# Performance work log

Hardware: AMD Instinct MI355X
Metric: run time of the kernel (lower is better)

## Reference

```python
import jax, jax.numpy as jnp
import numpy as np

DIM = 512
HEADS = 8
WS = 8  # window_size


def setup_inputs() -> dict:
    key = jax.random.key(0)
    ks = jax.random.split(key, 7)
    b, c, h, w = 4, DIM, 192, 192
    x = jax.random.normal(ks[0], (b, c, h, w), dtype=jnp.float32)
    # conv1x1 weights are [out, in] matrices (kernel dim squeezed)
    wq = jax.random.normal(ks[1], (DIM, DIM), dtype=jnp.float32) * 0.02
    wk = jax.random.normal(ks[2], (DIM, DIM), dtype=jnp.float32) * 0.02
    wv = jax.random.normal(ks[3], (DIM, DIM), dtype=jnp.float32) * 0.02
    wo = jax.random.normal(ks[4], (DIM, DIM), dtype=jnp.float32) * 0.02
    bo = jax.random.normal(ks[5], (DIM,), dtype=jnp.float32) * 0.02
    # learned per-head additive bias over window tokens (trunc_normal std=0.02)
    beta = jax.random.normal(ks[6], (HEADS, WS * WS, WS * WS), dtype=jnp.float32) * 0.02
    return {"x": x, "wq": wq, "wk": wk, "wv": wv, "wo": wo, "bo": bo, "beta": beta}


def reference(x, wq, wk, wv, wo, bo, beta):
    b, c, h, w = x.shape
    s = WS
    pad_r = (-w) % s
    pad_b = (-h) % s
    x = jnp.pad(x, ((0, 0), (0, 0), (0, pad_b), (0, pad_r)))
    H, W = h + pad_b, w + pad_r
    nh, nw = H // s, W // s
    n = s * s
    head_dim = c // HEADS
    scale = head_dim ** -0.5
    # window partition: (b, c, nh, s, nw, s) -> (b*nh*nw, c, n)
    xw = x.reshape(b, c, nh, s, nw, s).transpose(0, 2, 4, 1, 3, 5).reshape(b * nh * nw, c, n)
    B = xw.shape[0]
    q = jnp.einsum('oc,bcn->bon', wq, xw).reshape(B, HEADS, head_dim, n)
    k = jnp.einsum('oc,bcn->bon', wk, xw).reshape(B, HEADS, head_dim, n)
    v = jnp.einsum('oc,bcn->bon', wv, xw).reshape(B, HEADS, head_dim, n)
    attn = jnp.einsum('bhdn,bhdm->bhnm', q, k) * scale + beta  # [B,H,n,n]
    attn = jax.nn.softmax(attn, axis=-1)
    o = jnp.einsum('bhnm,bhdm->bhdn', attn, v).reshape(B, c, n)
    o = jnp.einsum('oc,bcn->bon', wo, o) + bo[None, :, None]
    # window merge back to image
    out = o.reshape(b, nh, nw, c, s, s).transpose(0, 3, 1, 4, 2, 5).reshape(b, c, H, W)
    return out[:, :, :h, :w]
```

## Files before the change

### kernel.cpp

```cpp
#include <hip/hip_runtime.h>

typedef unsigned short ushort_t;
typedef __attribute__((ext_vector_type(4))) float f32x4;
typedef __attribute__((ext_vector_type(8))) short short8;

__device__ __forceinline__ ushort_t f2bf(float f) {
  union { float f; unsigned u; } v; v.f = f;
  unsigned r = v.u + 0x7fffu + ((v.u >> 16) & 1u);
  return (ushort_t)(r >> 16);
}

__global__ __launch_bounds__(256) void cvt_w_k(const float* __restrict__ wq,
                                               const float* __restrict__ wk,
                                               const float* __restrict__ wv,
                                               const float* __restrict__ wo,
                                               ushort_t* __restrict__ dst) {
  int idx = (blockIdx.x * 256 + threadIdx.x) * 4;
  int m = idx >> 18;
  int off = idx & 0x3ffff;
  const float* s = (m == 0) ? wq : (m == 1) ? wk : (m == 2) ? wv : wo;
  float4 v = *(const float4*)(s + off);
  ushort4 o;
  o.x = f2bf(v.x); o.y = f2bf(v.y); o.z = f2bf(v.z); o.w = f2bf(v.w);
  *(ushort4*)(dst + idx) = o;
}

__global__ __launch_bounds__(256) void xpose_k(const float* __restrict__ x,
                                               ushort_t* __restrict__ xT) {
  __shared__ ushort_t tile[128 * 80];
  int bid = blockIdx.x;
  int win = bid >> 2, kc = bid & 3;
  int b = win / 576, rem = win % 576, wh = rem / 24, ww = rem % 24;
  int tid = threadIdx.x;
  {
    int c_l = tid >> 1, half = tid & 1;
    const float* xb = x + (((b * 512 + kc * 128 + c_l) * 192 + wh * 8) * 192 + ww * 8);
#pragma unroll
    for (int ii = 0; ii < 4; ++ii) {
      int i = half * 4 + ii;
      float4 v0 = *(const float4*)(xb + i * 192);
      float4 v1 = *(const float4*)(xb + i * 192 + 4);
      uint4 u;
      u.x = (unsigned)f2bf(v0.x) | ((unsigned)f2bf(v0.y) << 16);
      u.y = (unsigned)f2bf(v0.z) | ((unsigned)f2bf(v0.w) << 16);
      u.z = (unsigned)f2bf(v1.x) | ((unsigned)f2bf(v1.y) << 16);
      u.w = (unsigned)f2bf(v1.z) | ((unsigned)f2bf(v1.w) << 16);
      *(uint4*)&tile[c_l * 80 + i * 8] = u;
    }
  }
  __syncthreads();
  {
    int tok = tid >> 2, q = tid & 3;
    unsigned w[16];
#pragma unroll
    for (int k = 0; k < 16; ++k) {
      unsigned lo = tile[(q * 32 + 2 * k) * 80 + tok];
      unsigned hi = tile[(q * 32 + 2 * k + 1) * 80 + tok];
      w[k] = lo | (hi << 16);
    }
    ushort_t* d = xT + ((win * 64 + tok) * 512 + kc * 128 + q * 32);
#pragma unroll
    for (int s2 = 0; s2 < 4; ++s2) {
      uint4 u; u.x = w[s2 * 4 + 0]; u.y = w[s2 * 4 + 1]; u.z = w[s2 * 4 + 2]; u.w = w[s2 * 4 + 3];
      *(uint4*)(d + s2 * 8) = u;
    }
  }
}

__global__ __launch_bounds__(256) void attn_k(const ushort_t* __restrict__ xT,
                                              const ushort_t* __restrict__ wB,
                                              const float* __restrict__ beta,
                                              ushort_t* __restrict__ Og) {
  __shared__ ushort_t xws[64 * 136];
  __shared__ ushort_t qTs[64 * 72];
  __shared__ ushort_t kTs[64 * 72];
  __shared__ ushort_t vSs[64 * 72];
  int bid = blockIdx.x;
  int win = bid >> 3, h = bid & 7;
  int tid = threadIdx.x, lane = tid & 63, wid = tid >> 6;
  int l15 = lane & 15, l4 = lane >> 4;
  int t0 = win * 64;
  const ushort_t* wqh = wB + (h * 64) * 512;
  const ushort_t* wkh = wB + 262144 + (h * 64) * 512;
  const ushort_t* wvh = wB + 524288 + (h * 64) * 512;

  f32x4 z = {0.f, 0.f, 0.f, 0.f};
  f32x4 aq[4], ak[4], av[4];
#pragma unroll
  for (int i = 0; i < 4; ++i) { aq[i] = z; ak[i] = z; av[i] = z; }

  int stok = tid >> 2, sq = tid & 3;
  int dcol = wid * 16 + l15;
  for (int kcc = 0; kcc < 4; ++kcc) {
    {
      const uint4* src = (const uint4*)(xT + ((t0 + stok) * 512 + kcc * 128 + sq * 32));
      uint4* dstv = (uint4*)&xws[stok * 136 + sq * 32];
#pragma unroll
      for (int s2 = 0; s2 < 4; ++s2) dstv[s2] = src[s2];
    }
    __syncthreads();
#pragma unroll
    for (int kk = 0; kk < 4; ++kk) {
      int cg = kcc * 128 + kk * 32 + l4 * 8;
      short8 bq = *(const short8*)(wqh + dcol * 512 + cg);
      short8 bk = *(const short8*)(wkh + dcol * 512 + cg);
      short8 bv = *(const short8*)(wvh + dcol * 512 + cg);
#pragma unroll
      for (int nt = 0; nt < 4; ++nt) {
        short8 a = *(const short8*)&xws[(nt * 16 + l15) * 136 + kk * 32 + l4 * 8];
        aq[nt] = __builtin_amdgcn_mfma_f32_16x16x32_bf16(a, bq, aq[nt], 0, 0, 0);
        ak[nt] = __builtin_amdgcn_mfma_f32_16x16x32_bf16(a, bk, ak[nt], 0, 0, 0);
        av[nt] = __builtin_amdgcn_mfma_f32_16x16x32_bf16(a, bv, av[nt], 0, 0, 0);
      }
    }
    __syncthreads();
  }
#pragma unroll
  for (int nt = 0; nt < 4; ++nt) {
#pragma unroll
    for (int r = 0; r < 4; ++r) {
      int n = nt * 16 + l4 * 4 + r;
      int d = wid * 16 + l15;
      qTs[n * 72 + d] = f2bf(aq[nt][r]);
      kTs[n * 72 + d] = f2bf(ak[nt][r]);
    }
    uint2 u;
    u.x = (unsigned)f2bf(av[nt][0]) | ((unsigned)f2bf(av[nt][1]) << 16);
    u.y = (unsigned)f2bf(av[nt][2]) | ((unsigned)f2bf(av[nt][3]) << 16);
    *(uint2*)&vSs[(wid * 16 + l15) * 72 + nt * 16 + l4 * 4] = u;
  }
  __syncthreads();

  f32x4 sA[4];
#pragma unroll
  for (int i = 0; i < 4; ++i) sA[i] = z;
#pragma unroll
  for (int kk = 0; kk < 2; ++kk) {
    short8 aF = *(const short8*)&qTs[(wid * 16 + l15) * 72 + kk * 32 + l4 * 8];
#pragma unroll
    for (int mt = 0; mt < 4; ++mt) {
      short8 bF = *(const short8*)&kTs[(mt * 16 + l15) * 72 + kk * 32 + l4 * 8];
      sA[mt] = __builtin_amdgcn_mfma_f32_16x16x32_bf16(aF, bF, sA[mt], 0, 0, 0);
    }
  }
  const float* betah = beta + h * 4096;
  float p[4][4];
  float rmax[4] = {-1e30f, -1e30f, -1e30f, -1e30f};
#pragma unroll
  for (int mt = 0; mt < 4; ++mt)
#pragma unroll
    for (int r = 0; r < 4; ++r) {
      int n = wid * 16 + l4 * 4 + r;
      float val = sA[mt][r] * 0.125f + betah[n * 64 + mt * 16 + l15];
      p[mt][r] = val;
      rmax[r] = fmaxf(rmax[r], val);
    }
#pragma unroll
  for (int m = 1; m <= 8; m <<= 1)
#pragma unroll
    for (int r = 0; r < 4; ++r) rmax[r] = fmaxf(rmax[r], __shfl_xor(rmax[r], m, 64));
  float rsum[4] = {0.f, 0.f, 0.f, 0.f};
#pragma unroll
  for (int mt = 0; mt < 4; ++mt)
#pragma unroll
    for (int r = 0; r < 4; ++r) {
      p[mt][r] = __expf(p[mt][r] - rmax[r]);
      rsum[r] += p[mt][r];
    }
#pragma unroll
  for (int m = 1; m <= 8; m <<= 1)
#pragma unroll
    for (int r = 0; r < 4; ++r) rsum[r] += __shfl_xor(rsum[r], m, 64);
  float rinv[4];
#pragma unroll
  for (int r = 0; r < 4; ++r) rinv[r] = 1.f / rsum[r];
#pragma unroll
  for (int mt = 0; mt < 4; ++mt)
#pragma unroll
    for (int r = 0; r < 4; ++r)
      qTs[(wid * 16 + l4 * 4 + r) * 72 + mt * 16 + l15] = f2bf(p[mt][r] * rinv[r]);
  __syncthreads();

  f32x4 oA[4];
#pragma unroll
  for (int i = 0; i < 4; ++i) oA[i] = z;
#pragma unroll
  for (int kk = 0; kk < 2; ++kk) {
    short8 aF = *(const short8*)&qTs[(wid * 16 + l15) * 72 + kk * 32 + l4 * 8];
#pragma unroll
    for (int dt = 0; dt < 4; ++dt) {
      short8 bF = *(const short8*)&vSs[(dt * 16 + l15) * 72 + kk * 32 + l4 * 8];
      oA[dt] = __builtin_amdgcn_mfma_f32_16x16x32_bf16(aF, bF, oA[dt], 0, 0, 0);
    }
  }
#pragma unroll
  for (int dt = 0; dt < 4; ++dt)
#pragma unroll
    for (int r = 0; r < 4; ++r) {
      int n = wid * 16 + l4 * 4 + r;
      Og[(t0 + n) * 512 + h * 64 + dt * 16 + l15] = f2bf(oA[dt][r]);
    }
}

__global__ __launch_bounds__(256) void proj_k(const ushort_t* __restrict__ Og,
                                              const ushort_t* __restrict__ woB,
                                              const float* __restrict__ bo,
                                              float* __restrict__ out) {
  __shared__ ushort_t ows[64 * 136];
  int bid = blockIdx.x;
  int win = bid >> 1, mo = (bid & 1) * 256;
  int b = win / 576, rem = win % 576, wh = rem / 24, ww = rem % 24;
  int tid = threadIdx.x, lane = tid & 63, wid = tid >> 6;
  int l15 = lane & 15, l4 = lane >> 4;
  int t0 = win * 64;
  f32x4 z = {0.f, 0.f, 0.f, 0.f};
  f32x4 acc[4][4];
#pragma unroll
  for (int i = 0; i < 4; ++i)
#pragma unroll
    for (int j = 0; j < 4; ++j) acc[i][j] = z;
  int stok = tid >> 2, sq = tid & 3;
  for (int kcc = 0; kcc < 4; ++kcc) {
    {
      const uint4* src = (const uint4*)(Og + ((t0 + stok) * 512 + kcc * 128 + sq * 32));
      uint4* dstv = (uint4*)&ows[stok * 136 + sq * 32];
#pragma unroll
      for (int s2 = 0; s2 < 4; ++s2) dstv[s2] = src[s2];
    }
    __syncthreads();
#pragma unroll
    for (int kk = 0; kk < 4; ++kk) {
      short8 bF[4];
#pragma unroll
      for (int nt = 0; nt < 4; ++nt)
        bF[nt] = *(const short8*)&ows[(nt * 16 + l15) * 136 + kk * 32 + l4 * 8];
      int cg = kcc * 128 + kk * 32 + l4 * 8;
#pragma unroll
      for (int mt = 0; mt < 4; ++mt) {
        int orow = mo + wid * 64 + mt * 16 + l15;
        short8 aF = *(const short8*)(woB + orow * 512 + cg);
#pragma unroll
        for (int nt = 0; nt < 4; ++nt)
          acc[mt][nt] = __builtin_amdgcn_mfma_f32_16x16x32_bf16(aF, bF[nt], acc[mt][nt], 0, 0, 0);
      }
    }
    __syncthreads();
  }
#pragma unroll
  for (int mt = 0; mt < 4; ++mt) {
#pragma unroll
    for (int r = 0; r < 4; ++r) {
      int o = mo + wid * 64 + mt * 16 + l4 * 4 + r;
      float bias = bo[o];
#pragma unroll
      for (int nt = 0; nt < 4; ++nt) {
        int tok = nt * 16 + l15;
        int i = tok >> 3, j = tok & 7;
        out[((b * 512 + o) * 192 + wh * 8 + i) * 192 + ww * 8 + j] = acc[mt][nt][r] + bias;
      }
    }
  }
}

extern "C" void kernel_launch(void* const* d_in, const int* in_sizes, int n_in,
                              void* d_out, int out_size, void* d_ws, size_t ws_size,
                              hipStream_t stream) {
  const float* x    = (const float*)d_in[0];
  const float* wq   = (const float*)d_in[1];
  const float* wk   = (const float*)d_in[2];
  const float* wv   = (const float*)d_in[3];
  const float* wo   = (const float*)d_in[4];
  const float* bo   = (const float*)d_in[5];
  const float* beta = (const float*)d_in[6];

  ushort_t* wB = (ushort_t*)d_ws;
  ushort_t* Og = (ushort_t*)((char*)d_ws + (size_t)4 * 262144 * 2);
  ushort_t* xT = (ushort_t*)d_out;

  cvt_w_k<<<1024, 256, 0, stream>>>(wq, wk, wv, wo, wB);
  xpose_k<<<2304 * 4, 256, 0, stream>>>(x, xT);
  attn_k<<<2304 * 8, 256, 0, stream>>>(xT, wB, beta, Og);
  proj_k<<<2304 * 2, 256, 0, stream>>>(Og, wB + 3 * 262144, bo, (float*)d_out);
}
```

Before: 1.024 ms.

## Process all heads per window in one block, loading window activations once

```diff
diff --git a/kernel.cpp b/kernel.cpp
--- a/kernel.cpp
+++ b/kernel.cpp
@@ -67,139 +67,143 @@
   }
 }
 
-__global__ __launch_bounds__(256) void attn_k(const ushort_t* __restrict__ xT,
-                                              const ushort_t* __restrict__ wB,
-                                              const float* __restrict__ beta,
-                                              ushort_t* __restrict__ Og) {
-  __shared__ ushort_t xws[64 * 136];
-  __shared__ ushort_t qTs[64 * 72];
-  __shared__ ushort_t kTs[64 * 72];
-  __shared__ ushort_t vSs[64 * 72];
-  int bid = blockIdx.x;
-  int win = bid >> 3, h = bid & 7;
+__global__ __launch_bounds__(512) void qkv_attn_k(const ushort_t* __restrict__ xT,
+                                                  const ushort_t* __restrict__ wB,
+                                                  const float* __restrict__ beta,
+                                                  ushort_t* __restrict__ Og) {
+  __shared__ ushort_t xws[64 * 520];
+  __shared__ ushort_t qs[2][64 * 72];
+  __shared__ ushort_t ks[2][64 * 72];
+  __shared__ ushort_t vs[2][64 * 72];
+  int win = blockIdx.x;
+  int t0 = win * 64;
   int tid = threadIdx.x, lane = tid & 63, wid = tid >> 6;
   int l15 = lane & 15, l4 = lane >> 4;
-  int t0 = win * 64;
-  const ushort_t* wqh = wB + (h * 64) * 512;
-  const ushort_t* wkh = wB + 262144 + (h * 64) * 512;
-  const ushort_t* wvh = wB + 524288 + (h * 64) * 512;
-
-  f32x4 z = {0.f, 0.f, 0.f, 0.f};
-  f32x4 aq[4], ak[4], av[4];
-#pragma unroll
-  for (int i = 0; i < 4; ++i) { aq[i] = z; ak[i] = z; av[i] = z; }
-
-  int stok = tid >> 2, sq = tid & 3;
-  int dcol = wid * 16 + l15;
-  for (int kcc = 0; kcc < 4; ++kcc) {
-    {
-      const uint4* src = (const uint4*)(xT + ((t0 + stok) * 512 + kcc * 128 + sq * 32));
-      uint4* dstv = (uint4*)&xws[stok * 136 + sq * 32];
-#pragma unroll
-      for (int s2 = 0; s2 < 4; ++s2) dstv[s2] = src[s2];
-    }
-    __syncthreads();
-#pragma unroll
-    for (int kk = 0; kk < 4; ++kk) {
-      int cg = kcc * 128 + kk * 32 + l4 * 8;
-      short8 bq = *(const short8*)(wqh + dcol * 512 + cg);
-      short8 bk = *(const short8*)(wkh + dcol * 512 + cg);
-      short8 bv = *(const short8*)(wvh + dcol * 512 + cg);
+
+  {
+    int token = tid >> 3, cb = (tid & 7) * 64;
+    const uint4* src = (const uint4*)(xT + (size_t)(t0 + token) * 512 + cb);
+    uint4* dst = (uint4*)&xws[token * 520 + cb];
+#pragma unroll
+    for (int s2 = 0; s2 < 8; ++s2) dst[s2] = src[s2];
+  }
+  __syncthreads();
+
+  const f32x4 z = {0.f, 0.f, 0.f, 0.f};
+
+  for (int hcc = 0; hcc < 4; ++hcc) {
+    f32x4 aq[4], ak[4], av[4];
+#pragma unroll
+    for (int i = 0; i < 4; ++i) { aq[i] = z; ak[i] = z; av[i] = z; }
+    int ocol = hcc * 128 + wid * 16 + l15;
+    const ushort_t* wqr = wB + (size_t)ocol * 512;
+    const ushort_t* wkr = wB + 262144 + (size_t)ocol * 512;
+    const ushort_t* wvr = wB + 524288 + (size_t)ocol * 512;
+#pragma unroll
+    for (int kk = 0; kk < 16; ++kk) {
+      int cg = kk * 32 + l4 * 8;
+      short8 bq = *(const short8*)(wqr + cg);
+      short8 bk = *(const short8*)(wkr + cg);
+      short8 bv = *(const short8*)(wvr + cg);
 #pragma unroll
       for (int nt = 0; nt < 4; ++nt) {
-        short8 a = *(const short8*)&xws[(nt * 16 + l15) * 136 + kk * 32 + l4 * 8];
+        short8 a = *(const short8*)&xws[(nt * 16 + l15) * 520 + cg];
         aq[nt] = __builtin_amdgcn_mfma_f32_16x16x32_bf16(a, bq, aq[nt], 0, 0, 0);
         ak[nt] = __builtin_amdgcn_mfma_f32_16x16x32_bf16(a, bk, ak[nt], 0, 0, 0);
         av[nt] = __builtin_amdgcn_mfma_f32_16x16x32_bf16(a, bv, av[nt], 0, 0, 0);
       }
     }
-    __syncthreads();
-  }
-#pragma unroll
-  for (int nt = 0; nt < 4; ++nt) {
-#pragma unroll
-    for (int r = 0; r < 4; ++r) {
-      int n = nt * 16 + l4 * 4 + r;
-      int d = wid * 16 + l15;
-      qTs[n * 72 + d] = f2bf(aq[nt][r]);
-      kTs[n * 72 + d] = f2bf(ak[nt][r]);
-    }
-    uint2 u;
-    u.x = (unsigned)f2bf(av[nt][0]) | ((unsigned)f2bf(av[nt][1]) << 16);
-    u.y = (unsigned)f2bf(av[nt][2]) | ((unsigned)f2bf(av[nt][3]) << 16);
-    *(uint2*)&vSs[(wid * 16 + l15) * 72 + nt * 16 + l4 * 4] = u;
-  }
-  __syncthreads();
-
-  f32x4 sA[4];
-#pragma unroll
-  for (int i = 0; i < 4; ++i) sA[i] = z;
-#pragma unroll
-  for (int kk = 0; kk < 2; ++kk) {
-    short8 aF = *(const short8*)&qTs[(wid * 16 + l15) * 72 + kk * 32 + l4 * 8];
-#pragma unroll
-    for (int mt = 0; mt < 4; ++mt) {
-      short8 bF = *(const short8*)&kTs[(mt * 16 + l15) * 72 + kk * 32 + l4 * 8];
-      sA[mt] = __builtin_amdgcn_mfma_f32_16x16x32_bf16(aF, bF, sA[mt], 0, 0, 0);
-    }
-  }
-  const float* betah = beta + h * 4096;
-  float p[4][4];
-  float rmax[4] = {-1e30f, -1e30f, -1e30f, -1e30f};
-#pragma unroll
-  for (int mt = 0; mt < 4; ++mt)
-#pragma unroll
-    for (int r = 0; r < 4; ++r) {
-      int n = wid * 16 + l4 * 4 + r;
-      float val = sA[mt][r] * 0.125f + betah[n * 64 + mt * 16 + l15];
-      p[mt][r] = val;
-      rmax[r] = fmaxf(rmax[r], val);
-    }
-#pragma unroll
-  for (int m = 1; m <= 8; m <<= 1)
-#pragma unroll
-    for (int r = 0; r < 4; ++r) rmax[r] = fmaxf(rmax[r], __shfl_xor(rmax[r], m, 64));
-  float rsum[4] = {0.f, 0.f, 0.f, 0.f};
-#pragma unroll
-  for (int mt = 0; mt < 4; ++mt)
-#pragma unroll
-    for (int r = 0; r < 4; ++r) {
-      p[mt][r] = __expf(p[mt][r] - rmax[r]);
-      rsum[r] += p[mt][r];
-    }
-#pragma unroll
-  for (int m = 1; m <= 8; m <<= 1)
-#pragma unroll
-    for (int r = 0; r < 4; ++r) rsum[r] += __shfl_xor(rsum[r], m, 64);
-  float rinv[4];
-#pragma unroll
-  for (int r = 0; r < 4; ++r) rinv[r] = 1.f / rsum[r];
-#pragma unroll
-  for (int mt = 0; mt < 4; ++mt)
-#pragma unroll
-    for (int r = 0; r < 4; ++r)
-      qTs[(wid * 16 + l4 * 4 + r) * 72 + mt * 16 + l15] = f2bf(p[mt][r] * rinv[r]);
-  __syncthreads();
-
-  f32x4 oA[4];
-#pragma unroll
-  for (int i = 0; i < 4; ++i) oA[i] = z;
-#pragma unroll
-  for (int kk = 0; kk < 2; ++kk) {
-    short8 aF = *(const short8*)&qTs[(wid * 16 + l15) * 72 + kk * 32 + l4 * 8];
-#pragma unroll
-    for (int dt = 0; dt < 4; ++dt) {
-      short8 bF = *(const short8*)&vSs[(dt * 16 + l15) * 72 + kk * 32 + l4 * 8];
-      oA[dt] = __builtin_amdgcn_mfma_f32_16x16x32_bf16(aF, bF, oA[dt], 0, 0, 0);
-    }
-  }
-#pragma unroll
-  for (int dt = 0; dt < 4; ++dt)
-#pragma unroll
-    for (int r = 0; r < 4; ++r) {
-      int n = wid * 16 + l4 * 4 + r;
-      Og[(t0 + n) * 512 + h * 64 + dt * 16 + l15] = f2bf(oA[dt][r]);
-    }
+    int hw = wid >> 2;
+    int dd = (wid * 16 + l15) & 63;
+#pragma unroll
+    for (int nt = 0; nt < 4; ++nt) {
+#pragma unroll
+      for (int r = 0; r < 4; ++r) {
+        int n = nt * 16 + l4 * 4 + r;
+        qs[hw][n * 72 + dd] = f2bf(aq[nt][r]);
+        ks[hw][n * 72 + dd] = f2bf(ak[nt][r]);
+      }
+      uint2 u;
+      u.x = (unsigned)f2bf(av[nt][0]) | ((unsigned)f2bf(av[nt][1]) << 16);
+      u.y = (unsigned)f2bf(av[nt][2]) | ((unsigned)f2bf(av[nt][3]) << 16);
+      *(uint2*)&vs[hw][dd * 72 + nt * 16 + l4 * 4] = u;
+    }
+    __syncthreads();
+
+    int hh = wid >> 2, rowg = wid & 3;
+    int h = hcc * 2 + hh;
+    f32x4 sA[4];
+#pragma unroll
+    for (int i = 0; i < 4; ++i) sA[i] = z;
+#pragma unroll
+    for (int kk = 0; kk < 2; ++kk) {
+      short8 aF = *(const short8*)&qs[hh][(rowg * 16 + l15) * 72 + kk * 32 + l4 * 8];
+#pragma unroll
+      for (int mt = 0; mt < 4; ++mt) {
+        short8 bF = *(const short8*)&ks[hh][(mt * 16 + l15) * 72 + kk * 32 + l4 * 8];
+        sA[mt] = __builtin_amdgcn_mfma_f32_16x16x32_bf16(aF, bF, sA[mt], 0, 0, 0);
+      }
+    }
+    const float* betah = beta + h * 4096;
+    float p[4][4];
+    float rmax[4] = {-1e30f, -1e30f, -1e30f, -1e30f};
+#pragma unroll
+    for (int mt = 0; mt < 4; ++mt)
+#pragma unroll
+      for (int r = 0; r < 4; ++r) {
+        int n = rowg * 16 + l4 * 4 + r;
+        float val = sA[mt][r] * 0.125f + betah[n * 64 + mt * 16 + l15];
+        p[mt][r] = val;
+        rmax[r] = fmaxf(rmax[r], val);
+      }
+#pragma unroll
+    for (int m = 1; m <= 8; m <<= 1)
+#pragma unroll
+      for (int r = 0; r < 4; ++r) rmax[r] = fmaxf(rmax[r], __shfl_xor(rmax[r], m, 64));
+    float rsum[4] = {0.f, 0.f, 0.f, 0.f};
+#pragma unroll
+    for (int mt = 0; mt < 4; ++mt)
+#pragma unroll
+      for (int r = 0; r < 4; ++r) {
+        p[mt][r] = __expf(p[mt][r] - rmax[r]);
+        rsum[r] += p[mt][r];
+      }
+#pragma unroll
+    for (int m = 1; m <= 8; m <<= 1)
+#pragma unroll
+      for (int r = 0; r < 4; ++r) rsum[r] += __shfl_xor(rsum[r], m, 64);
+    float rinv[4];
+#pragma unroll
+    for (int r = 0; r < 4; ++r) rinv[r] = 1.f / rsum[r];
+    __syncthreads();
+#pragma unroll
+    for (int mt = 0; mt < 4; ++mt)
+#pragma unroll
+      for (int r = 0; r < 4; ++r)
+        qs[hh][(rowg * 16 + l4 * 4 + r) * 72 + mt * 16 + l15] = f2bf(p[mt][r] * rinv[r]);
+    __syncthreads();
+
+    f32x4 oA[4];
+#pragma unroll
+    for (int i = 0; i < 4; ++i) oA[i] = z;
+#pragma unroll
+    for (int kk = 0; kk < 2; ++kk) {
+      short8 aF = *(const short8*)&qs[hh][(rowg * 16 + l15) * 72 + kk * 32 + l4 * 8];
+#pragma unroll
+      for (int dt = 0; dt < 4; ++dt) {
+        short8 bF = *(const short8*)&vs[hh][(dt * 16 + l15) * 72 + kk * 32 + l4 * 8];
+        oA[dt] = __builtin_amdgcn_mfma_f32_16x16x32_bf16(aF, bF, oA[dt], 0, 0, 0);
+      }
+    }
+#pragma unroll
+    for (int dt = 0; dt < 4; ++dt)
+#pragma unroll
+      for (int r = 0; r < 4; ++r) {
+        int n = rowg * 16 + l4 * 4 + r;
+        Og[(size_t)(t0 + n) * 512 + h * 64 + dt * 16 + l15] = f2bf(oA[dt][r]);
+      }
+    __syncthreads();
+  }
 }
 
 __global__ __launch_bounds__(256) void proj_k(const ushort_t* __restrict__ Og,
@@ -279,6 +283,6 @@
 
   cvt_w_k<<<1024, 256, 0, stream>>>(wq, wk, wv, wo, wB);
   xpose_k<<<2304 * 4, 256, 0, stream>>>(x, xT);
-  attn_k<<<2304 * 8, 256, 0, stream>>>(xT, wB, beta, Og);
+  qkv_attn_k<<<2304, 512, 0, stream>>>(xT, wB, beta, Og);
   proj_k<<<2304 * 2, 256, 0, stream>>>(Og, wB + 3 * 262144, bo, (float*)d_out);
 }
```

After: 991.0 us. 1.03x faster.

## Split QKV projection into a large-tile GEMM and batch-chunk the pipeline

Applied to the files above, without the earlier changes.

```diff
diff --git a/kernel.cpp b/kernel.cpp
--- a/kernel.cpp
+++ b/kernel.cpp
@@ -26,15 +26,15 @@
 }
 
 __global__ __launch_bounds__(256) void xpose_k(const float* __restrict__ x,
-                                               ushort_t* __restrict__ xT) {
+                                               ushort_t* __restrict__ xT, int b0) {
   __shared__ ushort_t tile[128 * 80];
   int bid = blockIdx.x;
-  int win = bid >> 2, kc = bid & 3;
-  int b = win / 576, rem = win % 576, wh = rem / 24, ww = rem % 24;
+  int winl = bid >> 2, kc = bid & 3;
+  int b = b0 + winl / 576, rem = winl % 576, wh = rem / 24, ww = rem % 24;
   int tid = threadIdx.x;
   {
     int c_l = tid >> 1, half = tid & 1;
-    const float* xb = x + (((b * 512 + kc * 128 + c_l) * 192 + wh * 8) * 192 + ww * 8);
+    const float* xb = x + ((((size_t)b * 512 + kc * 128 + c_l) * 192 + wh * 8) * 192 + ww * 8);
 #pragma unroll
     for (int ii = 0; ii < 4; ++ii) {
       int i = half * 4 + ii;
@@ -58,7 +58,7 @@
       unsigned hi = tile[(q * 32 + 2 * k + 1) * 80 + tok];
       w[k] = lo | (hi << 16);
     }
-    ushort_t* d = xT + ((win * 64 + tok) * 512 + kc * 128 + q * 32);
+    ushort_t* d = xT + ((size_t)(winl * 64 + tok) * 512 + kc * 128 + q * 32);
 #pragma unroll
     for (int s2 = 0; s2 < 4; ++s2) {
       uint4 u; u.x = w[s2 * 4 + 0]; u.y = w[s2 * 4 + 1]; u.z = w[s2 * 4 + 2]; u.w = w[s2 * 4 + 3];
@@ -67,79 +67,126 @@
   }
 }
 
-__global__ __launch_bounds__(256) void attn_k(const ushort_t* __restrict__ xT,
-                                              const ushort_t* __restrict__ wB,
-                                              const float* __restrict__ beta,
-                                              ushort_t* __restrict__ Og) {
-  __shared__ ushort_t xws[64 * 136];
-  __shared__ ushort_t qTs[64 * 72];
-  __shared__ ushort_t kTs[64 * 72];
-  __shared__ ushort_t vSs[64 * 72];
+__global__ __launch_bounds__(256) void qkv_k(const ushort_t* __restrict__ xT,
+                                             const ushort_t* __restrict__ wB,
+                                             ushort_t* __restrict__ Og) {
+  __shared__ ushort_t As[128 * 72];
+  __shared__ ushort_t Bs[128 * 72];
   int bid = blockIdx.x;
-  int win = bid >> 3, h = bid & 7;
+  int cwg = gridDim.x >> 3;
+  int wg = (bid & 7) * cwg + (bid >> 3);
+  int mt = wg / 12, nt = wg % 12;
+  int t0 = mt * 128;
+  int tid = threadIdx.x, lane = tid & 63, wid = tid >> 6;
+  int wr = wid >> 1, wc = wid & 1;
+  int l15 = lane & 15, l4 = lane >> 4;
+  const ushort_t* Bsrc = wB + (size_t)(nt * 128) * 512;
+
+  const f32x4 z = {0.f, 0.f, 0.f, 0.f};
+  f32x4 acc[4][4];
+#pragma unroll
+  for (int i = 0; i < 4; ++i)
+#pragma unroll
+    for (int j = 0; j < 4; ++j) acc[i][j] = z;
+
+  int srow[4], sslot[4];
+#pragma unroll
+  for (int c = 0; c < 4; ++c) { int u = c * 256 + tid; srow[c] = u >> 3; sslot[c] = u & 7; }
+
+  uint4 ga[4], gb[4];
+#pragma unroll
+  for (int c = 0; c < 4; ++c) {
+    ga[c] = *(const uint4*)&xT[(size_t)(t0 + srow[c]) * 512 + sslot[c] * 8];
+    gb[c] = *(const uint4*)&Bsrc[(size_t)srow[c] * 512 + sslot[c] * 8];
+  }
+
+  for (int ks = 0; ks < 8; ++ks) {
+    __syncthreads();
+#pragma unroll
+    for (int c = 0; c < 4; ++c) {
+      *(uint4*)&As[srow[c] * 72 + sslot[c] * 8] = ga[c];
+      *(uint4*)&Bs[srow[c] * 72 + sslot[c] * 8] = gb[c];
+    }
+    if (ks < 7) {
+      int ko = (ks + 1) * 64;
+#pragma unroll
+      for (int c = 0; c < 4; ++c) {
+        ga[c] = *(const uint4*)&xT[(size_t)(t0 + srow[c]) * 512 + ko + sslot[c] * 8];
+        gb[c] = *(const uint4*)&Bsrc[(size_t)srow[c] * 512 + ko + sslot[c] * 8];
+      }
+    }
+    __syncthreads();
+#pragma unroll
+    for (int kk = 0; kk < 2; ++kk) {
+      short8 aF[4], bF[4];
+#pragma unroll
+      for (int mi = 0; mi < 4; ++mi)
+        aF[mi] = *(const short8*)&As[(wr * 64 + mi * 16 + l15) * 72 + kk * 32 + l4 * 8];
+#pragma unroll
+      for (int ni = 0; ni < 4; ++ni)
+        bF[ni] = *(const short8*)&Bs[(wc * 64 + ni * 16 + l15) * 72 + kk * 32 + l4 * 8];
+#pragma unroll
+      for (int mi = 0; mi < 4; ++mi)
+#pragma unroll
+        for (int ni = 0; ni < 4; ++ni)
+          acc[mi][ni] = __builtin_amdgcn_mfma_f32_16x16x32_bf16(aF[mi], bF[ni], acc[mi][ni], 0, 0, 0);
+    }
+  }
+#pragma unroll
+  for (int mi = 0; mi < 4; ++mi)
+#pragma unroll
+    for (int rr = 0; rr < 4; ++rr) {
+      size_t row = (size_t)(t0 + wr * 64 + mi * 16 + l4 * 4 + rr) * 1536;
+      int cb = nt * 128 + wc * 64 + l15;
+#pragma unroll
+      for (int ni = 0; ni < 4; ++ni)
+        Og[row + cb + ni * 16] = f2bf(acc[mi][ni][rr]);
+    }
+}
+
+__global__ __launch_bounds__(256) void attn2_k(const ushort_t* __restrict__ Og,
+                                               const float* __restrict__ beta,
+                                               ushort_t* __restrict__ O) {
+  __shared__ ushort_t qS[64 * 72], kS[64 * 72], vT[64 * 72], pS[64 * 72];
+  int bid = blockIdx.x;
+  int winl = bid >> 3, h = bid & 7;
+  int t0 = winl * 64;
   int tid = threadIdx.x, lane = tid & 63, wid = tid >> 6;
   int l15 = lane & 15, l4 = lane >> 4;
-  int t0 = win * 64;
-  const ushort_t* wqh = wB + (h * 64) * 512;
-  const ushort_t* wkh = wB + 262144 + (h * 64) * 512;
-  const ushort_t* wvh = wB + 524288 + (h * 64) * 512;
-
-  f32x4 z = {0.f, 0.f, 0.f, 0.f};
-  f32x4 aq[4], ak[4], av[4];
-#pragma unroll
-  for (int i = 0; i < 4; ++i) { aq[i] = z; ak[i] = z; av[i] = z; }
-
-  int stok = tid >> 2, sq = tid & 3;
-  int dcol = wid * 16 + l15;
-  for (int kcc = 0; kcc < 4; ++kcc) {
-    {
-      const uint4* src = (const uint4*)(xT + ((t0 + stok) * 512 + kcc * 128 + sq * 32));
-      uint4* dstv = (uint4*)&xws[stok * 136 + sq * 32];
-#pragma unroll
-      for (int s2 = 0; s2 < 4; ++s2) dstv[s2] = src[s2];
-    }
-    __syncthreads();
-#pragma unroll
-    for (int kk = 0; kk < 4; ++kk) {
-      int cg = kcc * 128 + kk * 32 + l4 * 8;
-      short8 bq = *(const short8*)(wqh + dcol * 512 + cg);
-      short8 bk = *(const short8*)(wkh + dcol * 512 + cg);
-      short8 bv = *(const short8*)(wvh + dcol * 512 + cg);
-#pragma unroll
-      for (int nt = 0; nt < 4; ++nt) {
-        short8 a = *(const short8*)&xws[(nt * 16 + l15) * 136 + kk * 32 + l4 * 8];
-        aq[nt] = __builtin_amdgcn_mfma_f32_16x16x32_bf16(a, bq, aq[nt], 0, 0, 0);
-        ak[nt] = __builtin_amdgcn_mfma_f32_16x16x32_bf16(a, bk, ak[nt], 0, 0, 0);
-        av[nt] = __builtin_amdgcn_mfma_f32_16x16x32_bf16(a, bv, av[nt], 0, 0, 0);
-      }
-    }
-    __syncthreads();
-  }
-#pragma unroll
-  for (int nt = 0; nt < 4; ++nt) {
-#pragma unroll
-    for (int r = 0; r < 4; ++r) {
-      int n = nt * 16 + l4 * 4 + r;
-      int d = wid * 16 + l15;
-      qTs[n * 72 + d] = f2bf(aq[nt][r]);
-      kTs[n * 72 + d] = f2bf(ak[nt][r]);
-    }
-    uint2 u;
-    u.x = (unsigned)f2bf(av[nt][0]) | ((unsigned)f2bf(av[nt][1]) << 16);
-    u.y = (unsigned)f2bf(av[nt][2]) | ((unsigned)f2bf(av[nt][3]) << 16);
-    *(uint2*)&vSs[(wid * 16 + l15) * 72 + nt * 16 + l4 * 4] = u;
+
+  {
+    int m = tid & 63, dg = tid >> 6;
+    const ushort_t* base = Og + (size_t)(t0 + m) * 1536 + h * 64 + dg * 16;
+    uint4 vq0 = *(const uint4*)(base);
+    uint4 vq1 = *(const uint4*)(base + 8);
+    uint4 vk0 = *(const uint4*)(base + 512);
+    uint4 vk1 = *(const uint4*)(base + 520);
+    uint4 vv0 = *(const uint4*)(base + 1024);
+    uint4 vv1 = *(const uint4*)(base + 1032);
+    *(uint4*)&qS[m * 72 + dg * 16] = vq0;
+    *(uint4*)&qS[m * 72 + dg * 16 + 8] = vq1;
+    *(uint4*)&kS[m * 72 + dg * 16] = vk0;
+    *(uint4*)&kS[m * 72 + dg * 16 + 8] = vk1;
+    int dbase = (dg * 16) * 72 + m;
+#define VW(word, j0) \
+    vT[dbase + (j0) * 72] = (ushort_t)((word) & 0xffffu); \
+    vT[dbase + ((j0) + 1) * 72] = (ushort_t)((word) >> 16);
+    VW(vv0.x, 0) VW(vv0.y, 2) VW(vv0.z, 4) VW(vv0.w, 6)
+    VW(vv1.x, 8) VW(vv1.y, 10) VW(vv1.z, 12) VW(vv1.w, 14)
+#undef VW
   }
   __syncthreads();
 
+  const f32x4 z = {0.f, 0.f, 0.f, 0.f};
   f32x4 sA[4];
 #pragma unroll
   for (int i = 0; i < 4; ++i) sA[i] = z;
 #pragma unroll
   for (int kk = 0; kk < 2; ++kk) {
-    short8 aF = *(const short8*)&qTs[(wid * 16 + l15) * 72 + kk * 32 + l4 * 8];
+    short8 aF = *(const short8*)&qS[(wid * 16 + l15) * 72 + kk * 32 + l4 * 8];
 #pragma unroll
     for (int mt = 0; mt < 4; ++mt) {
-      short8 bF = *(const short8*)&kTs[(mt * 16 + l15) * 72 + kk * 32 + l4 * 8];
+      short8 bF = *(const short8*)&kS[(mt * 16 + l15) * 72 + kk * 32 + l4 * 8];
       sA[mt] = __builtin_amdgcn_mfma_f32_16x16x32_bf16(aF, bF, sA[mt], 0, 0, 0);
     }
   }
@@ -178,18 +225,17 @@
   for (int mt = 0; mt < 4; ++mt)
 #pragma unroll
     for (int r = 0; r < 4; ++r)
-      qTs[(wid * 16 + l4 * 4 + r) * 72 + mt * 16 + l15] = f2bf(p[mt][r] * rinv[r]);
-  __syncthreads();
+      pS[(wid * 16 + l4 * 4 + r) * 72 + mt * 16 + l15] = f2bf(p[mt][r] * rinv[r]);
 
   f32x4 oA[4];
 #pragma unroll
   for (int i = 0; i < 4; ++i) oA[i] = z;
 #pragma unroll
   for (int kk = 0; kk < 2; ++kk) {
-    short8 aF = *(const short8*)&qTs[(wid * 16 + l15) * 72 + kk * 32 + l4 * 8];
+    short8 aF = *(const short8*)&pS[(wid * 16 + l15) * 72 + kk * 32 + l4 * 8];
 #pragma unroll
     for (int dt = 0; dt < 4; ++dt) {
-      short8 bF = *(const short8*)&vSs[(dt * 16 + l15) * 72 + kk * 32 + l4 * 8];
+      short8 bF = *(const short8*)&vT[(dt * 16 + l15) * 72 + kk * 32 + l4 * 8];
       oA[dt] = __builtin_amdgcn_mfma_f32_16x16x32_bf16(aF, bF, oA[dt], 0, 0, 0);
     }
   }
@@ -198,68 +244,88 @@
 #pragma unroll
     for (int r = 0; r < 4; ++r) {
       int n = wid * 16 + l4 * 4 + r;
-      Og[(t0 + n) * 512 + h * 64 + dt * 16 + l15] = f2bf(oA[dt][r]);
-    }
-}
-
-__global__ __launch_bounds__(256) void proj_k(const ushort_t* __restrict__ Og,
-                                              const ushort_t* __restrict__ woB,
-                                              const float* __restrict__ bo,
-                                              float* __restrict__ out) {
-  __shared__ ushort_t ows[64 * 136];
+      O[(size_t)(t0 + n) * 512 + h * 64 + dt * 16 + l15] = f2bf(oA[dt][r]);
+    }
+}
+
+__global__ __launch_bounds__(256) void proj_k2(const ushort_t* __restrict__ O,
+                                               const ushort_t* __restrict__ woB,
+                                               const float* __restrict__ bo,
+                                               float* __restrict__ out, int w0) {
+  __shared__ ushort_t As[128 * 72];
+  __shared__ ushort_t Bs[128 * 72];
   int bid = blockIdx.x;
-  int win = bid >> 1, mo = (bid & 1) * 256;
+  int cwg = gridDim.x >> 3;
+  int wg = (bid & 7) * cwg + (bid >> 3);
+  int nn = wg >> 2, mm = wg & 3;
+  int tid = threadIdx.x, lane = tid & 63, wid = tid >> 6;
+  int wr = wid >> 1, wc = wid & 1;
+  int l15 = lane & 15, l4 = lane >> 4;
+  const ushort_t* Asrc = woB + (size_t)(mm * 128) * 512;
+  const ushort_t* Bsrc = O + (size_t)(nn * 128) * 512;
+
+  const f32x4 z = {0.f, 0.f, 0.f, 0.f};
+  f32x4 acc[4][4];
+#pragma unroll
+  for (int i = 0; i < 4; ++i)
+#pragma unroll
+    for (int j = 0; j < 4; ++j) acc[i][j] = z;
+
+  int srow[4], sslot[4];
+#pragma unroll
+  for (int c = 0; c < 4; ++c) { int u = c * 256 + tid; srow[c] = u >> 3; sslot[c] = u & 7; }
+  uint4 ga[4], gb[4];
+#pragma unroll
+  for (int c = 0; c < 4; ++c) {
+    ga[c] = *(const uint4*)&Asrc[(size_t)srow[c] * 512 + sslot[c] * 8];
+    gb[c] = *(const uint4*)&Bsrc[(size_t)srow[c] * 512 + sslot[c] * 8];
+  }
+  for (int ks = 0; ks < 8; ++ks) {
+    __syncthreads();
+#pragma unroll
+    for (int c = 0; c < 4; ++c) {
+      *(uint4*)&As[srow[c] * 72 + sslot[c] * 8] = ga[c];
+      *(uint4*)&Bs[srow[c] * 72 + sslot[c] * 8] = gb[c];
+    }
+    if (ks < 7) {
+      int ko = (ks + 1) * 64;
+#pragma unroll
+      for (int c = 0; c < 4; ++c) {
+        ga[c] = *(const uint4*)&Asrc[(size_t)srow[c] * 512 + ko + sslot[c] * 8];
+        gb[c] = *(const uint4*)&Bsrc[(size_t)srow[c] * 512 + ko + sslot[c] * 8];
+      }
+    }
+    __syncthreads();
+#pragma unroll
+    for (int kk = 0; kk < 2; ++kk) {
+      short8 aF[4], bF[4];
+#pragma unroll
+      for (int mi = 0; mi < 4; ++mi)
+        aF[mi] = *(const short8*)&As[(wr * 64 + mi * 16 + l15) * 72 + kk * 32 + l4 * 8];
+#pragma unroll
+      for (int ni = 0; ni < 4; ++ni)
+        bF[ni] = *(const short8*)&Bs[(wc * 64 + ni * 16 + l15) * 72 + kk * 32 + l4 * 8];
+#pragma unroll
+      for (int mi = 0; mi < 4; ++mi)
+#pragma unroll
+        for (int ni = 0; ni < 4; ++ni)
+          acc[mi][ni] = __builtin_amdgcn_mfma_f32_16x16x32_bf16(aF[mi], bF[ni], acc[mi][ni], 0, 0, 0);
+    }
+  }
+  int win = w0 + nn * 2 + wc;
   int b = win / 576, rem = win % 576, wh = rem / 24, ww = rem % 24;
-  int tid = threadIdx.x, lane = tid & 63, wid = tid >> 6;
-  int l15 = lane & 15, l4 = lane >> 4;
-  int t0 = win * 64;
-  f32x4 z = {0.f, 0.f, 0.f, 0.f};
-  f32x4 acc[4][4];
-#pragma unroll
-  for (int i = 0; i < 4; ++i)
-#pragma unroll
-    for (int j = 0; j < 4; ++j) acc[i][j] = z;
-  int stok = tid >> 2, sq = tid & 3;
-  for (int kcc = 0; kcc < 4; ++kcc) {
-    {
-      const uint4* src = (const uint4*)(Og + ((t0 + stok) * 512 + kcc * 128 + sq * 32));
-      uint4* dstv = (uint4*)&ows[stok * 136 + sq * 32];
-#pragma unroll
-      for (int s2 = 0; s2 < 4; ++s2) dstv[s2] = src[s2];
-    }
-    __syncthreads();
-#pragma unroll
-    for (int kk = 0; kk < 4; ++kk) {
-      short8 bF[4];
-#pragma unroll
-      for (int nt = 0; nt < 4; ++nt)
-        bF[nt] = *(const short8*)&ows[(nt * 16 + l15) * 136 + kk * 32 + l4 * 8];
-      int cg = kcc * 128 + kk * 32 + l4 * 8;
-#pragma unroll
-      for (int mt = 0; mt < 4; ++mt) {
-        int orow = mo + wid * 64 + mt * 16 + l15;
-        short8 aF = *(const short8*)(woB + orow * 512 + cg);
-#pragma unroll
-        for (int nt = 0; nt < 4; ++nt)
-          acc[mt][nt] = __builtin_amdgcn_mfma_f32_16x16x32_bf16(aF, bF[nt], acc[mt][nt], 0, 0, 0);
-      }
-    }
-    __syncthreads();
-  }
-#pragma unroll
-  for (int mt = 0; mt < 4; ++mt) {
-#pragma unroll
-    for (int r = 0; r < 4; ++r) {
-      int o = mo + wid * 64 + mt * 16 + l4 * 4 + r;
+  int jj = l15 & 7, ib = l15 >> 3;
+#pragma unroll
+  for (int mi = 0; mi < 4; ++mi)
+#pragma unroll
+    for (int rr = 0; rr < 4; ++rr) {
+      int o = mm * 128 + wr * 64 + mi * 16 + l4 * 4 + rr;
       float bias = bo[o];
-#pragma unroll
-      for (int nt = 0; nt < 4; ++nt) {
-        int tok = nt * 16 + l15;
-        int i = tok >> 3, j = tok & 7;
-        out[((b * 512 + o) * 192 + wh * 8 + i) * 192 + ww * 8 + j] = acc[mt][nt][r] + bias;
-      }
-    }
-  }
+      size_t ob = (((size_t)b * 512 + o) * 192 + wh * 8) * 192 + ww * 8 + jj;
+#pragma unroll
+      for (int ni = 0; ni < 4; ++ni)
+        out[ob + (size_t)(ni * 2 + ib) * 192] = acc[mi][ni][rr] + bias;
+    }
 }
 
 extern "C" void kernel_launch(void* const* d_in, const int* in_sizes, int n_in,
@@ -274,11 +340,23 @@
   const float* beta = (const float*)d_in[6];
 
   ushort_t* wB = (ushort_t*)d_ws;
-  ushort_t* Og = (ushort_t*)((char*)d_ws + (size_t)4 * 262144 * 2);
-  ushort_t* xT = (ushort_t*)d_out;
-
   cvt_w_k<<<1024, 256, 0, stream>>>(wq, wk, wv, wo, wB);
-  xpose_k<<<2304 * 4, 256, 0, stream>>>(x, xT);
-  attn_k<<<2304 * 8, 256, 0, stream>>>(xT, wB, beta, Og);
-  proj_k<<<2304 * 2, 256, 0, stream>>>(Og, wB + 3 * 262144, bo, (float*)d_out);
-}
+
+  int nchunk = (ws_size >= (size_t)606076928) ? 1 : 4;
+  int nb = 4 / nchunk;
+  int nwin = nb * 576;
+  int Tc = nwin * 64;
+  char* base = (char*)d_ws + (size_t)2097152;
+  ushort_t* xT = (ushort_t*)base;
+  ushort_t* Og = (ushort_t*)(base + (size_t)Tc * 512 * 2);
+  ushort_t* O  = xT;
+
+  for (int ch = 0; ch < nchunk; ++ch) {
+    int b0 = ch * nb;
+    xpose_k<<<nwin * 4, 256, 0, stream>>>(x, xT, b0);
+    qkv_k<<<(Tc / 128) * 12, 256, 0, stream>>>(xT, wB, Og);
+    attn2_k<<<nwin * 8, 256, 0, stream>>>(Og, beta, O);
+    proj_k2<<<(Tc / 128) * 4, 256, 0, stream>>>(O, wB + 3 * 262144, bo,
+                                                (float*)d_out, b0 * 576);
+  }
+}
```

Result: slower. 1.948 ms (+90.3%).
